# Kernel optimization log

Hardware: AMD Instinct MI355X
Metric: run time of the kernel (lower is better)

## Reference

```python
import jax, jax.numpy as jnp
import numpy as np

B, T, F = 64, 96, 32          # batch, window_size, num_features
H_ENC, H_DEC = 128, 128       # encoder / decoder hidden sizes


def _lstm_cell(x, h, c, k, r, b):
    # Keras LSTMCell math: gates ordered i, f, g(candidate), o
    z = x @ k + h @ r + b
    i, f, g, o = jnp.split(z, 4, axis=-1)
    i = jax.nn.sigmoid(i)
    f = jax.nn.sigmoid(f)
    g = jnp.tanh(g)
    o = jax.nn.sigmoid(o)
    c_new = f * c + i * g
    h_new = o * jnp.tanh(c_new)
    return h_new, c_new


def setup_inputs() -> dict:
    key = jax.random.key(0)
    ks = jax.random.split(key, 20)
    s = 0.05
    d = {
        "inputs": jax.random.normal(ks[0], (B, T, F), jnp.float32),
        # encoder LSTMCell (input dim = F)
        "enc_k": jax.random.normal(ks[1], (F, 4 * H_ENC), jnp.float32) * s,
        "enc_r": jax.random.normal(ks[2], (H_ENC, 4 * H_ENC), jnp.float32) * s,
        "enc_b": jnp.zeros((4 * H_ENC,), jnp.float32),
        # encoder attention MLP: in = 2*H_ENC + T -> H_ENC -> 1
        "ae_w1": jax.random.normal(ks[3], (2 * H_ENC + T, H_ENC), jnp.float32) * s,
        "ae_b1": jnp.zeros((H_ENC,), jnp.float32),
        "ae_w2": jax.random.normal(ks[4], (H_ENC, 1), jnp.float32) * s,
        "ae_b2": jnp.zeros((1,), jnp.float32),
        # decoder LSTMCell (input dim = H_DEC, the fc output)
        "dec_k": jax.random.normal(ks[5], (H_DEC, 4 * H_DEC), jnp.float32) * s,
        "dec_r": jax.random.normal(ks[6], (H_DEC, 4 * H_DEC), jnp.float32) * s,
        "dec_b": jnp.zeros((4 * H_DEC,), jnp.float32),
        # decoder attention MLP: in = 2*H_DEC + H_ENC -> H_ENC -> 1
        "ad_w1": jax.random.normal(ks[7], (2 * H_DEC + H_ENC, H_ENC), jnp.float32) * s,
        "ad_b1": jnp.zeros((H_ENC,), jnp.float32),
        "ad_w2": jax.random.normal(ks[8], (H_ENC, 1), jnp.float32) * s,
        "ad_b2": jnp.zeros((1,), jnp.float32),
        # fc: (context H_ENC + y_prev 1) -> H_DEC
        "fc_w": jax.random.normal(ks[9], (H_ENC + 1, H_DEC), jnp.float32) * s,
        "fc_b": jnp.zeros((H_DEC,), jnp.float32),
        # fc_final: (d_n H_DEC + context H_ENC) -> F
        "ff_w": jax.random.normal(ks[10], (H_DEC + H_ENC, F), jnp.float32) * s,
        "ff_b": jnp.zeros((F,), jnp.float32),
    }
    return d


def reference(inputs, enc_k, enc_r, enc_b, ae_w1, ae_b1, ae_w2, ae_b2,
              dec_k, dec_r, dec_b, ad_w1, ad_b1, ad_w2, ad_b2,
              fc_w, fc_b, ff_w, ff_b):
    b, t, f = inputs.shape
    h_enc = enc_r.shape[0]
    h_dec = dec_r.shape[0]
    x_perm = jnp.transpose(inputs, (0, 2, 1))  # [B, F, T] (constant over time)

    # ---------------- encoder: input-attention LSTM over time ----------------
    def enc_step(carry, x_t):
        h, s = carry  # each [B, H_enc]
        hb = jnp.broadcast_to(h[:, None, :], (b, f, h_enc))
        sb = jnp.broadcast_to(s[:, None, :], (b, f, h_enc))
        cat = jnp.concatenate([hb, sb, x_perm], axis=2)       # [B, F, 2H+T]
        e = jnp.tanh(cat @ ae_w1 + ae_b1) @ ae_w2 + ae_b2     # [B, F, 1]
        alpha = jax.nn.softmax(e[..., 0], axis=1)             # [B, F]
        x_tilde = alpha * x_t                                 # [B, F]
        h, s = _lstm_cell(x_tilde, h, s, enc_k, enc_r, enc_b)
        return (h, s), h

    init = (jnp.zeros((b, h_enc), inputs.dtype), jnp.zeros((b, h_enc), inputs.dtype))
    _, h_all = jax.lax.scan(enc_step, init, jnp.transpose(inputs, (1, 0, 2)))
    x_encoded = jnp.transpose(h_all, (1, 0, 2))               # [B, T, H_enc]

    # ---------------- decoder: temporal-attention LSTM over time -------------
    y_prev = inputs[:, :, -1]                                 # [B, T]

    def dec_step(carry, y_t):
        d, c, _ = carry
        db = jnp.broadcast_to(d[:, None, :], (b, t, h_dec))
        cb = jnp.broadcast_to(c[:, None, :], (b, t, h_dec))
        cat = jnp.concatenate([db, cb, x_encoded], axis=2)    # [B, T, 2Hd+He]
        e = jnp.tanh(cat @ ad_w1 + ad_b1) @ ad_w2 + ad_b2     # [B, T, 1]
        beta = jax.nn.softmax(e[..., 0], axis=1)              # [B, T]
        ctx = jnp.einsum("bt,bth->bh", beta, x_encoded)       # [B, H_enc]
        y_tilde = jnp.concatenate([ctx, y_t[:, None]], axis=1) @ fc_w + fc_b
        d, c = _lstm_cell(y_tilde, d, c, dec_k, dec_r, dec_b)
        return (d, c, ctx), None

    init_d = (jnp.zeros((b, h_dec), inputs.dtype),
              jnp.zeros((b, h_dec), inputs.dtype),
              jnp.zeros((b, h_enc), inputs.dtype))
    (d_n, _, ctx), _ = jax.lax.scan(dec_step, init_d, jnp.transpose(y_prev, (1, 0)))

    y_pred = jnp.concatenate([d_n, ctx], axis=1) @ ff_w + ff_b  # [B, F]
    return y_pred[:, None, :]                                   # [B, 1, F]
```

## Files before the change

### kernel.cpp

```cpp
#include <hip/hip_runtime.h>

#define TT 96
#define FF 32
#define HH 128
#define G4 512
#define LOG2E 1.4426950408889634f

typedef _Float16 h2 __attribute__((ext_vector_type(2)));

__device__ __forceinline__ float fexp2(float x){ return __builtin_amdgcn_exp2f(x); }
__device__ __forceinline__ float frcp(float x){ return __builtin_amdgcn_rcpf(x); }
__device__ __forceinline__ float fsigmoid(float x){ return frcp(1.0f + fexp2(-LOG2E*x)); }
__device__ __forceinline__ float ftanh(float x){
    float u = fexp2(2.0f*LOG2E*x);
    return 1.0f - 2.0f*frcp(1.0f + u);
}
__device__ __forceinline__ h2 pk(float a, float b){
    h2 r; r.x = (_Float16)a; r.y = (_Float16)b; return r;
}
__device__ __forceinline__ unsigned pku(float a, float b){
    return __builtin_bit_cast(unsigned, pk(a, b));
}
__device__ __forceinline__ h2 u2h(unsigned v){ return __builtin_bit_cast(h2, v); }
__device__ __forceinline__ float fdot2(h2 a, h2 b, float c){
#if __has_builtin(__builtin_amdgcn_fdot2)
    return __builtin_amdgcn_fdot2(a, b, c, false);
#else
    return c + (float)a.x*(float)b.x + (float)a.y*(float)b.y;
#endif
}

__global__ __launch_bounds__(256) void k_prep(const float* __restrict__ fc_w,
                                              const float* __restrict__ fc_b,
                                              const float* __restrict__ dec_k,
                                              const float* __restrict__ dec_b,
                                              h2* __restrict__ Gp,
                                              float* __restrict__ gy,
                                              float* __restrict__ gb){
    int blk = blockIdx.x, tid = threadIdx.x;
    int u0 = tid, u1 = tid + 256;
    if (blk < 16){
        float a0[8], a1[8];
        #pragma unroll
        for (int r = 0; r < 8; ++r){ a0[r] = 0.f; a1[r] = 0.f; }
        for (int m = 0; m < 128; ++m){
            float d0 = dec_k[m*G4 + u0], d1 = dec_k[m*G4 + u1];
            #pragma unroll
            for (int r = 0; r < 8; ++r){
                float w = fc_w[(blk*8 + r)*HH + m];
                a0[r] += w * d0; a1[r] += w * d1;
            }
        }
        #pragma unroll
        for (int c = 0; c < 4; ++c){
            Gp[(blk*G4 + u0)*4 + c] = pk(a0[2*c], a0[2*c+1]);
            Gp[(blk*G4 + u1)*4 + c] = pk(a1[2*c], a1[2*c+1]);
        }
    } else if (blk == 16){
        float a0 = 0.f, a1 = 0.f;
        for (int m = 0; m < 128; ++m){
            float w = fc_w[128*HH + m];
            a0 += w * dec_k[m*G4 + u0]; a1 += w * dec_k[m*G4 + u1];
        }
        gy[u0] = a0; gy[u1] = a1;
    } else {
        float a0 = 0.f, a1 = 0.f;
        for (int m = 0; m < 128; ++m){
            float w = fc_b[m];
            a0 += w * dec_k[m*G4 + u0]; a1 += w * dec_k[m*G4 + u1];
        }
        gb[u0] = a0 + dec_b[u0]; gb[u1] = a1 + dec_b[u1];
    }
}

__global__ __launch_bounds__(1024, 1)
void k_enc(const float* __restrict__ inputs,
           const float* __restrict__ enc_k,
           const float* __restrict__ enc_r,
           const float* __restrict__ enc_b,
           const float* __restrict__ ae_w1,
           const float* __restrict__ ae_b1,
           const float* __restrict__ ae_w2,
           const float* __restrict__ ad_w1,
           float* __restrict__ ws_xenc,
           float* __restrict__ ws_xept){
    extern __shared__ float lds[];
    uint4* KLH4 = (uint4*)lds;
    float* XPJT = lds + 8192;
    float* XIN  = lds + 12416;
    float* HST  = lds + 15488;
    float* PP   = lds + 15744;
    float* PPZ  = lds + 16768;
    float* PE   = lds + 17792;
    float* W2E  = lds + 17920;
    float* AB1E = lds + 18048;
    h2*    HSP  = (h2*)(lds + 18176);
    h2*    XTP  = (h2*)(lds + 18240);
    uint4* WAE4 = (uint4*)(lds + 18256);
    _Float16* XEF = (_Float16*)(lds + 34640);

    const int b = blockIdx.x, tid = threadIdx.x;
    const int u = tid & 511, hf = tid >> 9;
    const int j7 = tid & 127, g8 = tid >> 7;
    const float* xin_g = inputs + b*TT*FF;

    for (int i = tid; i < TT*FF; i += 1024) XIN[i] = xin_g[i];
    for (int i = tid; i < 2048; i += 1024){
        int f8 = i >> 9, uu = i & 511;
        uint4 q;
        q.x = pku(enc_k[(f8*8+0)*G4+uu], enc_k[(f8*8+1)*G4+uu]);
        q.y = pku(enc_k[(f8*8+2)*G4+uu], enc_k[(f8*8+3)*G4+uu]);
        q.z = pku(enc_k[(f8*8+4)*G4+uu], enc_k[(f8*8+5)*G4+uu]);
        q.w = pku(enc_k[(f8*8+6)*G4+uu], enc_k[(f8*8+7)*G4+uu]);
        KLH4[i] = q;
    }
    for (int i = tid; i < 4096; i += 1024){
        int j = i & 127, i4g = i >> 7;
        int kbase = (i4g >> 2)*32 + (i4g & 3)*8;
        uint4 wv;
        wv.x = pku(ae_w1[(kbase+0)*HH + j], ae_w1[(kbase+1)*HH + j]);
        wv.y = pku(ae_w1[(kbase+2)*HH + j], ae_w1[(kbase+3)*HH + j]);
        wv.z = pku(ae_w1[(kbase+4)*HH + j], ae_w1[(kbase+5)*HH + j]);
        wv.w = pku(ae_w1[(kbase+6)*HH + j], ae_w1[(kbase+7)*HH + j]);
        WAE4[i] = wv;
    }
    if (tid < 128){ W2E[tid] = ae_w2[tid]; AB1E[tid] = ae_b1[tid]; HSP[tid] = pk(0.f, 0.f); }
    if (tid < 256) HST[tid] = 0.f;

    h2 rp_e[32];
    #pragma unroll
    for (int i = 0; i < 32; ++i)
        rp_e[i] = pk(enc_r[(hf*64 + 2*i)*G4 + u], enc_r[(hf*64 + 2*i+1)*G4 + u]);
    const float eb = (hf == 0) ? enc_b[u] : 0.f;
    __syncthreads();

    {
        int j = tid & 127, fh = tid >> 7;
        float a0=0.f, a1=0.f, a2=0.f, a3=0.f;
        for (int t = 0; t < TT; ++t){
            float w = ae_w1[(256 + t)*HH + j];
            const float* xr = &XIN[t*FF + fh*4];
            a0 += xr[0]*w; a1 += xr[1]*w; a2 += xr[2]*w; a3 += xr[3]*w;
        }
        XPJT[j*33 + fh*4 + 0] = a0;
        XPJT[j*33 + fh*4 + 1] = a1;
        XPJT[j*33 + fh*4 + 2] = a2;
        XPJT[j*33 + fh*4 + 3] = a3;
    }
    __syncthreads();

    const int f5 = tid & 31, jg5 = tid >> 5;
    float er_e[4], sumw2e = 0.f;
    #pragma unroll
    for (int i = 0; i < 4; ++i){
        er_e[i] = fexp2(2.0f*LOG2E * XPJT[(jg5*4 + i)*33 + f5]);
        sumw2e += W2E[jg5*4 + i];
    }

    const uint4* HSP4 = (const uint4*)HSP;
    const uint4* XTP4 = (const uint4*)XTP;

    for (int t = 0; t < TT; ++t){
        {
            float a0 = 0.f, a1 = 0.f;
            #pragma unroll
            for (int i4 = 0; i4 < 4; ++i4){
                uint4 q  = HSP4[g8*4 + i4];
                uint4 wv = WAE4[(g8*4 + i4)*128 + j7];
                a0 = fdot2(u2h(q.x), u2h(wv.x), a0);
                a1 = fdot2(u2h(q.y), u2h(wv.y), a1);
                a0 = fdot2(u2h(q.z), u2h(wv.z), a0);
                a1 = fdot2(u2h(q.w), u2h(wv.w), a1);
            }
            PP[tid] = a0 + a1;
        }
        float z = eb;
        {
            float z2 = 0.f;
            #pragma unroll
            for (int i4 = 0; i4 < 8; ++i4){
                uint4 q = HSP4[hf*8 + i4];
                z  = fdot2(u2h(q.x), rp_e[i4*4+0], z);
                z2 = fdot2(u2h(q.y), rp_e[i4*4+1], z2);
                z  = fdot2(u2h(q.z), rp_e[i4*4+2], z);
                z2 = fdot2(u2h(q.w), rp_e[i4*4+3], z2);
            }
            z += z2;
        }
        __syncthreads();
        if (tid < 128){
            float s = AB1E[tid];
            #pragma unroll
            for (int g = 0; g < 8; ++g) s += PP[tid + 128*g];
            PE[tid] = fexp2(2.0f*LOG2E * s);
        }
        __syncthreads();
        {
            float acc2 = 0.f;
            #pragma unroll
            for (int i = 0; i < 4; ++i){
                float uu = PE[jg5*4 + i];
                float w  = W2E[jg5*4 + i];
                acc2 += w * frcp(fmaf(er_e[i], uu, 1.0f));
            }
            PP[tid] = sumw2e - 2.0f*acc2;
        }
        __syncthreads();
        if (tid < 32){
            float e = 0.f;
            #pragma unroll
            for (int g = 0; g < 32; ++g) e += PP[g*32 + tid];
            float p = fexp2(e * LOG2E);
            float ss = p;
            #pragma unroll
            for (int d = 16; d; d >>= 1) ss += __shfl_xor(ss, d, 32);
            float xt = p * frcp(ss) * XIN[t*FF + tid];
            float xt2 = __shfl_xor(xt, 1);
            if (!(tid & 1)) XTP[tid >> 1] = pk(xt, xt2);
        }
        __syncthreads();
        {
            float z2 = 0.f;
            #pragma unroll
            for (int c = 0; c < 2; ++c){
                int f8 = hf*2 + c;
                uint4 kq = KLH4[f8*512 + u];
                uint4 xq = XTP4[f8];
                z  = fdot2(u2h(kq.x), u2h(xq.x), z);
                z2 = fdot2(u2h(kq.y), u2h(xq.y), z2);
                z  = fdot2(u2h(kq.z), u2h(xq.z), z);
                z2 = fdot2(u2h(kq.w), u2h(xq.w), z2);
            }
            PPZ[hf*512 + u] = z + z2;
        }
        __syncthreads();
        if (tid < 128){
            int j = tid;
            float zi = PPZ[j]       + PPZ[512 + j];
            float zf = PPZ[128 + j] + PPZ[640 + j];
            float zg = PPZ[256 + j] + PPZ[768 + j];
            float zo = PPZ[384 + j] + PPZ[896 + j];
            float iv = fsigmoid(zi);
            float fv = fsigmoid(zf);
            float gv = ftanh(zg);
            float ov = fsigmoid(zo);
            float cn = fv * HST[128 + j] + iv * gv;
            float hn = ov * ftanh(cn);
            HST[128 + j] = cn;
            HST[j] = hn;
            ws_xenc[(b*TT + t)*HH + j] = hn;
            XEF[t*HH + j] = (_Float16)hn;
            float hn2 = __shfl_xor(hn, 1);
            float cn2 = __shfl_xor(cn, 1);
            if (!(j & 1)){
                HSP[j >> 1]        = pk(hn, hn2);
                HSP[64 + (j >> 1)] = pk(cn, cn2);
            }
        }
        __syncthreads();
    }

    {
        int j = tid & 127, th = tid >> 7;
        float acc[12];
        #pragma unroll
        for (int i = 0; i < 12; ++i) acc[i] = 0.f;
        for (int k = 0; k < 128; ++k){
            float w = ad_w1[(256 + k)*HH + j];
            #pragma unroll
            for (int i = 0; i < 12; ++i)
                acc[i] += (float)XEF[(th*12 + i)*HH + k] * w;
        }
        #pragma unroll
        for (int i = 0; i < 12; ++i)
            ws_xept[(b*HH + j)*TT + th*12 + i] = acc[i];
    }
}

__global__ __launch_bounds__(1024, 1)
void k_dec(const float* __restrict__ inputs,
           const float* __restrict__ dec_r,
           const float* __restrict__ ad_w1,
           const float* __restrict__ ad_b1,
           const float* __restrict__ ad_w2,
           const float* __restrict__ ff_w,
           const float* __restrict__ ff_b,
           const h2* __restrict__ Gp,
           const float* __restrict__ gy,
           const float* __restrict__ gb,
           const float* __restrict__ ws_xenc,
           const float* __restrict__ ws_xept,
           float* __restrict__ out){
    extern __shared__ float lds[];
    uint4* XE4 = (uint4*)lds;
    uint4* WDC4= (uint4*)(lds + 6144);
    float* PP  = lds + 22528;
    float* PPZ = lds + 23552;
    float* PPA = lds + 24576;
    float* APJ = lds + 25600;
    float* DST = lds + 25728;
    float* CTX = lds + 25984;
    float* W2L = lds + 26112;
    float* YV  = lds + 26240;
    float* SCAL= lds + 26336;
    h2*    DCP = (h2*)(lds + 26344);
    h2*    CXP = (h2*)(lds + 26408);
    h2*    BEP = (h2*)(lds + 26440);

    const int b = blockIdx.x, tid = threadIdx.x;
    const int u = tid & 511, hf = tid >> 9;
    const int j = tid & 127, og = tid >> 7;

    {
        const float* xe_g = ws_xenc + b*TT*HH;
        for (int i = tid; i < 12*HH; i += 1024){
            int t8 = i >> 7, k = i & 127;
            uint4 qq;
            qq.x = pku(xe_g[(t8*8 + 0)*HH + k], xe_g[(t8*8 + 1)*HH + k]);
            qq.y = pku(xe_g[(t8*8 + 2)*HH + k], xe_g[(t8*8 + 3)*HH + k]);
            qq.z = pku(xe_g[(t8*8 + 4)*HH + k], xe_g[(t8*8 + 5)*HH + k]);
            qq.w = pku(xe_g[(t8*8 + 6)*HH + k], xe_g[(t8*8 + 7)*HH + k]);
            XE4[i] = qq;
        }
    }
    for (int i = tid; i < 4096; i += 1024){
        int jj = i & 127, i4g = i >> 7;
        int kbase = (i4g >> 2)*32 + (i4g & 3)*8;
        uint4 wv;
        wv.x = pku(ad_w1[(kbase+0)*HH + jj], ad_w1[(kbase+1)*HH + jj]);
        wv.y = pku(ad_w1[(kbase+2)*HH + jj], ad_w1[(kbase+3)*HH + jj]);
        wv.z = pku(ad_w1[(kbase+4)*HH + jj], ad_w1[(kbase+5)*HH + jj]);
        wv.w = pku(ad_w1[(kbase+6)*HH + jj], ad_w1[(kbase+7)*HH + jj]);
        WDC4[i] = wv;
    }
    if (tid < TT) YV[tid] = inputs[b*TT*FF + tid*FF + (FF-1)];
    if (tid < 128){ W2L[tid] = ad_w2[tid]; DCP[tid] = pk(0.f, 0.f); }
    if (tid < 256) DST[tid] = 0.f;

    h2 rp[32];
    #pragma unroll
    for (int i = 0; i < 32; ++i)
        rp[i] = pk(dec_r[(hf*64 + 2*i)*G4 + u], dec_r[(hf*64 + 2*i+1)*G4 + u]);

    uint4 Greg[8];
    {
        const uint4* GQ = (const uint4*)Gp;
        #pragma unroll
        for (int g = 0; g < 8; ++g) Greg[g] = GQ[(hf*8 + g)*G4 + u];
    }

    float er[16];
    {
        const float* xp_g = ws_xept + (b*HH + og*16)*TT + j;
        if (j < TT){
            #pragma unroll
            for (int i = 0; i < 16; ++i) er[i] = fexp2(2.0f*LOG2E * xp_g[i*TT]);
        } else {
            #pragma unroll
            for (int i = 0; i < 16; ++i) er[i] = 1.0f;
        }
    }

    const float gbr = gb[u], gyr = gy[u];
    const float ab1 = (tid < 128) ? ad_b1[tid] : 0.f;
    __syncthreads();

    float sumw2 = 0.f;
    #pragma unroll
    for (int i = 0; i < 16; ++i) sumw2 += W2L[og*16 + i];

    const uint4* DCP4 = (const uint4*)DCP;
    const uint4* CXP4 = (const uint4*)CXP;
    const uint4* BEP4 = (const uint4*)BEP;

    for (int t = 0; t < TT; ++t){
        float z = (hf == 0) ? (gbr + YV[t]*gyr) : 0.f;
        {
            float z2 = 0.f;
            #pragma unroll
            for (int i4 = 0; i4 < 8; ++i4){
                uint4 q = DCP4[hf*8 + i4];
                z  = fdot2(u2h(q.x), rp[i4*4+0], z);
                z2 = fdot2(u2h(q.y), rp[i4*4+1], z2);
                z  = fdot2(u2h(q.z), rp[i4*4+2], z);
                z2 = fdot2(u2h(q.w), rp[i4*4+3], z2);
            }
            z += z2;
        }
        {
            float s0 = 0.f, s1 = 0.f;
            #pragma unroll
            for (int i = 0; i < 4; ++i){
                uint4 dq = DCP4[og*4 + i];
                uint4 wv = WDC4[(og*4 + i)*128 + j];
                s0 = fdot2(u2h(dq.x), u2h(wv.x), s0);
                s1 = fdot2(u2h(dq.y), u2h(wv.y), s1);
                s0 = fdot2(u2h(dq.z), u2h(wv.z), s0);
                s1 = fdot2(u2h(dq.w), u2h(wv.w), s1);
            }
            PPA[og*128 + j] = s0 + s1;
        }
        __syncthreads();
        if (tid < 128){
            float s = ab1;
            #pragma unroll
            for (int g = 0; g < 8; ++g) s += PPA[tid + 128*g];
            APJ[tid] = fexp2(2.0f*LOG2E * s);
        }
        __syncthreads();
        {
            float acc = 0.f;
            if (j < TT){
                float acc2 = 0.f;
                #pragma unroll
                for (int q4 = 0; q4 < 4; ++q4){
                    float4 uj = *(const float4*)&APJ[og*16 + q4*4];
                    float4 wj = *(const float4*)&W2L[og*16 + q4*4];
                    acc2 += wj.x * frcp(fmaf(er[q4*4+0], uj.x, 1.0f));
                    acc2 += wj.y * frcp(fmaf(er[q4*4+1], uj.y, 1.0f));
                    acc2 += wj.z * frcp(fmaf(er[q4*4+2], uj.z, 1.0f));
                    acc2 += wj.w * frcp(fmaf(er[q4*4+3], uj.w, 1.0f));
                }
                acc = sumw2 - 2.0f*acc2;
            }
            PP[tid] = acc;
        }
        __syncthreads();
        if (tid < 64){
            float ea = 0.f;
            #pragma unroll
            for (int g = 0; g < 8; ++g) ea += PP[tid + 128*g];
            float pa = fexp2(ea * LOG2E);
            float pb = 0.f;
            if (tid < 32){
                float ebv = 0.f;
                #pragma unroll
                for (int g = 0; g < 8; ++g) ebv += PP[64 + tid + 128*g];
                pb = fexp2(ebv * LOG2E);
            }
            float ss = pa + pb;
            #pragma unroll
            for (int d = 32; d; d >>= 1) ss += __shfl_xor(ss, d, 64);
            float pa2 = __shfl_xor(pa, 1);
            float pb2 = __shfl_xor(pb, 1);
            if (!(tid & 1)){
                BEP[tid >> 1] = pk(pa, pa2);
                if (tid < 32) BEP[32 + (tid >> 1)] = pk(pb, pb2);
            }
            if (tid == 0) SCAL[0] = frcp(ss);
        }
        __syncthreads();
        if (tid < 128){
            float s0 = 0.f, s1 = 0.f;
            #pragma unroll
            for (int t8 = 0; t8 < 12; t8 += 2){
                uint4 xq0 = XE4[t8*HH + tid],     bb0 = BEP4[t8];
                uint4 xq1 = XE4[(t8+1)*HH + tid], bb1 = BEP4[t8+1];
                s0 = fdot2(u2h(xq0.x), u2h(bb0.x), s0);
                s1 = fdot2(u2h(xq0.y), u2h(bb0.y), s1);
                s0 = fdot2(u2h(xq0.z), u2h(bb0.z), s0);
                s1 = fdot2(u2h(xq0.w), u2h(bb0.w), s1);
                s0 = fdot2(u2h(xq1.x), u2h(bb1.x), s0);
                s1 = fdot2(u2h(xq1.y), u2h(bb1.y), s1);
                s0 = fdot2(u2h(xq1.z), u2h(bb1.z), s0);
                s1 = fdot2(u2h(xq1.w), u2h(bb1.w), s1);
            }
            float cv = (s0 + s1) * SCAL[0];
            CTX[tid] = cv;
            float cv2 = __shfl_xor(cv, 1);
            if (!(tid & 1)) CXP[tid >> 1] = pk(cv, cv2);
        }
        __syncthreads();
        {
            float z2 = 0.f;
            #pragma unroll
            for (int gi = 0; gi < 8; ++gi){
                uint4 q  = Greg[gi];
                uint4 cc = CXP4[hf*8 + gi];
                z  = fdot2(u2h(q.x), u2h(cc.x), z);
                z2 = fdot2(u2h(q.y), u2h(cc.y), z2);
                z  = fdot2(u2h(q.z), u2h(cc.z), z);
                z2 = fdot2(u2h(q.w), u2h(cc.w), z2);
            }
            PPZ[hf*512 + u] = z + z2;
        }
        __syncthreads();
        if (tid < 128){
            int jj = tid;
            float zi = PPZ[jj]       + PPZ[512 + jj];
            float zf = PPZ[128 + jj] + PPZ[640 + jj];
            float zg = PPZ[256 + jj] + PPZ[768 + jj];
            float zo = PPZ[384 + jj] + PPZ[896 + jj];
            float iv = fsigmoid(zi);
            float fv = fsigmoid(zf);
            float gv = ftanh(zg);
            float ov = fsigmoid(zo);
            float cn = fv * DST[128 + jj] + iv * gv;
            float hn = ov * ftanh(cn);
            DST[128 + jj] = cn;
            DST[jj] = hn;
            float hn2 = __shfl_xor(hn, 1);
            float cn2 = __shfl_xor(cn, 1);
            if (!(jj & 1)){
                DCP[jj >> 1]        = pk(hn, hn2);
                DCP[64 + (jj >> 1)] = pk(cn, cn2);
            }
        }
        __syncthreads();
    }

    {
        int jp = tid & 31, sg = tid >> 5;
        float a = 0.f;
        #pragma unroll
        for (int kk = 0; kk < 8; ++kk){
            int k = sg*8 + kk;
            float val = (k < 128) ? DST[k] : CTX[k - 128];
            a += val * ff_w[k*FF + jp];
        }
        PP[sg*32 + jp] = a;
    }
    __syncthreads();
    if (tid < 32){
        float o = ff_b[tid];
        #pragma unroll
        for (int s = 0; s < 32; ++s) o += PP[s*32 + tid];
        out[b*FF + tid] = o;
    }
}

extern "C" void kernel_launch(void* const* d_in, const int* in_sizes, int n_in,
                              void* d_out, int out_size, void* d_ws, size_t ws_size,
                              hipStream_t stream) {
    const float* inputs = (const float*)d_in[0];
    const float* enc_k  = (const float*)d_in[1];
    const float* enc_r  = (const float*)d_in[2];
    const float* enc_b  = (const float*)d_in[3];
    const float* ae_w1  = (const float*)d_in[4];
    const float* ae_b1  = (const float*)d_in[5];
    const float* ae_w2  = (const float*)d_in[6];
    const float* dec_k  = (const float*)d_in[8];
    const float* dec_r  = (const float*)d_in[9];
    const float* dec_b  = (const float*)d_in[10];
    const float* ad_w1  = (const float*)d_in[11];
    const float* ad_b1  = (const float*)d_in[12];
    const float* ad_w2  = (const float*)d_in[13];
    const float* fc_w   = (const float*)d_in[15];
    const float* fc_b   = (const float*)d_in[16];
    const float* ff_w   = (const float*)d_in[17];
    const float* ff_b   = (const float*)d_in[18];

    float* ws      = (float*)d_ws;
    float* ws_xenc = ws;
    float* ws_xept = ws + 786432;
    h2*    Gp      = (h2*)(ws + 1572864);
    float* gy      = ws + 1605632;
    float* gb      = ws + 1606144;

    hipFuncSetAttribute((const void*)k_enc, hipFuncAttributeMaxDynamicSharedMemorySize, 163136);
    hipFuncSetAttribute((const void*)k_dec, hipFuncAttributeMaxDynamicSharedMemorySize, 105888);

    k_prep<<<18, 256, 0, stream>>>(fc_w, fc_b, dec_k, dec_b, Gp, gy, gb);
    k_enc<<<64, 1024, 163136, stream>>>(inputs, enc_k, enc_r, enc_b, ae_w1, ae_b1, ae_w2,
                                        ad_w1, ws_xenc, ws_xept);
    k_dec<<<64, 1024, 105888, stream>>>(inputs, dec_r, ad_w1, ad_b1, ad_w2, ff_w, ff_b,
                                        Gp, gy, gb, ws_xenc, ws_xept, (float*)d_out);
}
```

Measured before the change: 792.1 us.

## Fold attention w2 weights into reciprocal terms and move recurrent dot into barrier gaps

The w2 weight is folded into the per-thread exponent and bias terms, so w/(1+e*u) becomes 1/(e*u/w + 1/w). This drops the shared-memory W2L loads and one multiply per term in the attention score loop. The recurrent h@R dot product is also split so threads 0-127 compute it before the first barrier while the rest compute it in the slot where the first 128 threads reduce PPA, balancing work across the barrier. Dividing by w2 is fragile if any weight is near zero, and 32 extra registers per thread are held.

```diff
diff --git a/kernel.cpp b/kernel.cpp
--- a/kernel.cpp
+++ b/kernel.cpp
@@ -334,7 +334,7 @@
         WDC4[i] = wv;
     }
     if (tid < TT) YV[tid] = inputs[b*TT*FF + tid*FF + (FF-1)];
-    if (tid < 128){ W2L[tid] = ad_w2[tid]; DCP[tid] = pk(0.f, 0.f); }
+    if (tid < 128) DCP[tid] = pk(0.f, 0.f);
     if (tid < 256) DST[tid] = 0.f;
 
     h2 rp[32];
@@ -349,15 +349,17 @@
         for (int g = 0; g < 8; ++g) Greg[g] = GQ[(hf*8 + g)*G4 + u];
     }
 
-    float er[16];
+    float erw[16], iw[16], sumw2 = 0.f;
     {
         const float* xp_g = ws_xept + (b*HH + og*16)*TT + j;
-        if (j < TT){
-            #pragma unroll
-            for (int i = 0; i < 16; ++i) er[i] = fexp2(2.0f*LOG2E * xp_g[i*TT]);
-        } else {
-            #pragma unroll
-            for (int i = 0; i < 16; ++i) er[i] = 1.0f;
+        #pragma unroll
+        for (int i = 0; i < 16; ++i){
+            float w2v = ad_w2[og*16 + i];
+            float ivv = 1.0f / w2v;
+            iw[i] = ivv;
+            sumw2 += w2v;
+            float xp = (j < TT) ? xp_g[i*TT] : 0.f;
+            erw[i] = fexp2(2.0f*LOG2E * xp) * ivv;
         }
     }
 
@@ -365,28 +367,12 @@
     const float ab1 = (tid < 128) ? ad_b1[tid] : 0.f;
     __syncthreads();
 
-    float sumw2 = 0.f;
-    #pragma unroll
-    for (int i = 0; i < 16; ++i) sumw2 += W2L[og*16 + i];
-
     const uint4* DCP4 = (const uint4*)DCP;
     const uint4* CXP4 = (const uint4*)CXP;
     const uint4* BEP4 = (const uint4*)BEP;
 
     for (int t = 0; t < TT; ++t){
         float z = (hf == 0) ? (gbr + YV[t]*gyr) : 0.f;
-        {
-            float z2 = 0.f;
-            #pragma unroll
-            for (int i4 = 0; i4 < 8; ++i4){
-                uint4 q = DCP4[hf*8 + i4];
-                z  = fdot2(u2h(q.x), rp[i4*4+0], z);
-                z2 = fdot2(u2h(q.y), rp[i4*4+1], z2);
-                z  = fdot2(u2h(q.z), rp[i4*4+2], z);
-                z2 = fdot2(u2h(q.w), rp[i4*4+3], z2);
-            }
-            z += z2;
-        }
         {
             float s0 = 0.f, s1 = 0.f;
             #pragma unroll
@@ -400,12 +386,35 @@
             }
             PPA[og*128 + j] = s0 + s1;
         }
+        if (tid < 128){
+            float z2 = 0.f;
+            #pragma unroll
+            for (int i4 = 0; i4 < 8; ++i4){
+                uint4 q = DCP4[hf*8 + i4];
+                z  = fdot2(u2h(q.x), rp[i4*4+0], z);
+                z2 = fdot2(u2h(q.y), rp[i4*4+1], z2);
+                z  = fdot2(u2h(q.z), rp[i4*4+2], z);
+                z2 = fdot2(u2h(q.w), rp[i4*4+3], z2);
+            }
+            z += z2;
+        }
         __syncthreads();
         if (tid < 128){
             float s = ab1;
             #pragma unroll
             for (int g = 0; g < 8; ++g) s += PPA[tid + 128*g];
             APJ[tid] = fexp2(2.0f*LOG2E * s);
+        } else {
+            float z2 = 0.f;
+            #pragma unroll
+            for (int i4 = 0; i4 < 8; ++i4){
+                uint4 q = DCP4[hf*8 + i4];
+                z  = fdot2(u2h(q.x), rp[i4*4+0], z);
+                z2 = fdot2(u2h(q.y), rp[i4*4+1], z2);
+                z  = fdot2(u2h(q.z), rp[i4*4+2], z);
+                z2 = fdot2(u2h(q.w), rp[i4*4+3], z2);
+            }
+            z += z2;
         }
         __syncthreads();
         {
@@ -415,11 +424,10 @@
                 #pragma unroll
                 for (int q4 = 0; q4 < 4; ++q4){
                     float4 uj = *(const float4*)&APJ[og*16 + q4*4];
-                    float4 wj = *(const float4*)&W2L[og*16 + q4*4];
-                    acc2 += wj.x * frcp(fmaf(er[q4*4+0], uj.x, 1.0f));
-                    acc2 += wj.y * frcp(fmaf(er[q4*4+1], uj.y, 1.0f));
-                    acc2 += wj.z * frcp(fmaf(er[q4*4+2], uj.z, 1.0f));
-                    acc2 += wj.w * frcp(fmaf(er[q4*4+3], uj.w, 1.0f));
+                    acc2 += frcp(fmaf(erw[q4*4+0], uj.x, iw[q4*4+0]));
+                    acc2 += frcp(fmaf(erw[q4*4+1], uj.y, iw[q4*4+1]));
+                    acc2 += frcp(fmaf(erw[q4*4+2], uj.z, iw[q4*4+2]));
+                    acc2 += frcp(fmaf(erw[q4*4+3], uj.w, iw[q4*4+3]));
                 }
                 acc = sumw2 - 2.0f*acc2;
             }
```

Result: faster. 699.3 us (-11.7%).
